# Performance work log

Measured on AMD Instinct MI355X. Metric: run time of the kernel, lower is better.

Reference implementation:

```python
import jax, jax.numpy as jnp
import numpy as np

B, N, FEAT = 4, 100000, 11
NUM_SP = 512  # superpoints per sample
H1, H2, H3, E = 128, 256, 512, 384


def setup_inputs() -> dict:
    key = jax.random.key(0)
    ks = jax.random.split(key, 10)
    s = 0.02
    return {
        "full_features": jax.random.normal(ks[0], (B, N, FEAT), dtype=jnp.float32),
        "full_super_indices": jax.random.randint(ks[1], (B, N), 0, NUM_SP, dtype=jnp.int32),
        "W1": jax.random.normal(ks[2], (H1, FEAT), dtype=jnp.float32) * s,
        "b1": jnp.zeros((H1,), jnp.float32),
        "W2": jax.random.normal(ks[3], (H2, H1), dtype=jnp.float32) * s,
        "b2": jnp.zeros((H2,), jnp.float32),
        "W3": jax.random.normal(ks[4], (H3, H3), dtype=jnp.float32) * s,
        "b3": jnp.zeros((H3,), jnp.float32),
        "W4": jax.random.normal(ks[5], (E, H3), dtype=jnp.float32) * s,
        "b4": jnp.zeros((E,), jnp.float32),
    }


def reference(full_features, full_super_indices, W1, b1, W2, b2, W3, b3, W4, b4):
    # Vectorized form of the per-superpoint mini-PointNet:
    # conv1x1 MLP on points, segment-max pool, concat global+local, MLP, segment-max.
    x = full_features.reshape(B * N, FEAT)
    # first_conv: Conv1d(feat,128,1) -> Conv1d(128,256,1), no activation in between
    h = x @ W1.T + b1
    h = h @ W2.T + b2                                   # [B*N, 256]
    # global segment ids (batch-offset superpoint ids)
    seg = (full_super_indices.astype(jnp.int32) + jnp.arange(B, dtype=jnp.int32)[:, None] * NUM_SP).reshape(-1)
    gmax = jax.ops.segment_max(h, seg, num_segments=B * NUM_SP)  # [B*S, 256]
    g = gmax[seg]                                       # broadcast global feature back to points
    feat = jnp.concatenate([g, h], axis=-1)             # [B*N, 512] (global first, as in torch.cat)
    # second_conv: Conv1d(512,512,1) -> ReLU -> Conv1d(512,E,1)
    y = jax.nn.relu(feat @ W3.T + b3)
    y = y @ W4.T + b4                                   # [B*N, E]
    out = jax.ops.segment_max(y, seg, num_segments=B * NUM_SP)
    return out.reshape(B, NUM_SP, E)
```

## Files before the change

### kernel.cpp

```cpp
#include <hip/hip_runtime.h>
#include <hip/hip_bf16.h>
#include <math.h>

#define BB    4
#define NN    100000
#define NFEAT 11
#define NSP   512
#define NSEG  (BB*NSP)
#define NPTS  (BB*NN)
#define H2    256
#define H3    512
#define EE    384
#define MT    64
#define GS    (MT*8)
#define MI_N  (MT/16)
#define MAXL  15
#define RSEG  512
#define MAXS  12
#define ENCNI 0x007FFFFFu

typedef __attribute__((ext_vector_type(8))) short short8;
typedef __attribute__((ext_vector_type(4))) float f32x4;

__device__ __forceinline__ ushort f2bf(float f) {
  unsigned u = __builtin_bit_cast(unsigned, f);
  unsigned r = (u + 0x7FFFu + ((u >> 16) & 1u)) >> 16;
  return (ushort)r;
}
__device__ __forceinline__ unsigned encf(float f) {
  unsigned u = __builtin_bit_cast(unsigned, f);
  return u ^ ((unsigned)((int)u >> 31) | 0x80000000u);
}
__device__ __forceinline__ float decf(unsigned e) {
  unsigned u = (e & 0x80000000u) ? (e ^ 0x80000000u) : ~e;
  return __builtin_bit_cast(float, u);
}

__global__ void zero_counts(int* __restrict__ counts, int* __restrict__ cursor) {
  int i = blockIdx.x * 256 + threadIdx.x;
  if (i < NSEG) { counts[i] = 0; cursor[i] = 0; }
}

__global__ void prep_init(const float* __restrict__ W1, const float* __restrict__ b1,
                          const float* __restrict__ W2, const float* __restrict__ b2,
                          const float* __restrict__ W3, const float* __restrict__ W4,
                          const int* __restrict__ sidx,
                          float* __restrict__ W12, float* __restrict__ b12,
                          float* __restrict__ W3gT, ushort* __restrict__ W3hP,
                          ushort* __restrict__ W4P,
                          int* __restrict__ counts,
                          unsigned* __restrict__ gmaxEnc, unsigned* __restrict__ out_enc) {
  int u = blockIdx.x * 256 + threadIdx.x;
  if (u < NSEG * EE) out_enc[u] = ENCNI;
  if (u < NSEG * H2) gmaxEnc[u] = ENCNI;
  if (u < NPTS) {
    int seg = sidx[u] + (u / NN) * NSP;
    atomicAdd(&counts[seg], 1);
  }

  if (u < H2 * NFEAT) {
    int c = u / NFEAT, f = u - c * NFEAT;
    float acc = 0.f;
    for (int j = 0; j < 128; ++j) acc += W2[c * 128 + j] * W1[j * NFEAT + f];
    W12[u] = acc;
  } else if (u < 3072) {
    int c = u - H2 * NFEAT;
    float acc = b2[c];
    for (int j = 0; j < 128; ++j) acc += W2[c * 128 + j] * b1[j];
    b12[c] = acc;
  } else if (u < 3072 + 131072) {
    int v = u - 3072;
    int c = v >> 9, o = v & 511;
    W3gT[v] = W3[o * H3 + c];
  } else if (u < 134144 + 16384) {
    int v = u - 134144;
    int ks = v >> 11, rem = v & 2047;
    int nt = rem >> 6, l = rem & 63;
    int n = nt * 16 + (l & 15);
    #pragma unroll
    for (int j = 0; j < 8; ++j) {
      int k = ks * 32 + (l >> 4) * 8 + j;
      W3hP[(size_t)v * 8 + j] = f2bf(W3[n * H3 + H2 + k]);
    }
  } else if (u < 150528 + 24576) {
    int v = u - 150528;
    int ks = v / 1536, rem = v - ks * 1536;
    int nt = rem >> 6, l = rem & 63;
    int n = nt * 16 + (l & 15);
    #pragma unroll
    for (int j = 0; j < 8; ++j) {
      int k = ks * 32 + (l >> 4) * 8 + j;
      W4P[(size_t)v * 8 + j] = f2bf(W4[n * H3 + k]);
    }
  }
}

__global__ void scan_kernel(const int* __restrict__ counts, int* __restrict__ offs) {
  __shared__ int buf[1024];
  int t = threadIdx.x;
  int c0 = counts[2 * t], c1 = counts[2 * t + 1];
  int s = c0 + c1;
  buf[t] = s;
  __syncthreads();
  for (int d = 1; d < 1024; d <<= 1) {
    int add = (t >= d) ? buf[t - d] : 0;
    __syncthreads();
    buf[t] += add;
    __syncthreads();
  }
  int incl = buf[t];
  int excl = incl - s;
  offs[2 * t] = excl;
  offs[2 * t + 1] = excl + c0;
  if (t == 1023) offs[2048] = incl;
}

__global__ void scatter_kernel(const int* __restrict__ sidx, const int* __restrict__ offs,
                               int* __restrict__ cursor, int* __restrict__ perm,
                               int* __restrict__ segp) {
  int i = blockIdx.x * blockDim.x + threadIdx.x;
  if (i < NPTS) {
    int seg = sidx[i] + (i / NN) * NSP;
    int pos = offs[seg] + atomicAdd(&cursor[seg], 1);
    perm[pos] = i;
    segp[pos] = seg;
  }
}

template <bool STOREH>
__global__ __launch_bounds__(512) void gmax_kernel(
    const float* __restrict__ x, const int* __restrict__ perm,
    const int* __restrict__ segp,
    const float* __restrict__ W12, const float* __restrict__ b12,
    unsigned* __restrict__ gmaxEnc, ushort* __restrict__ hG) {
  __shared__ float xs[RSEG * NFEAT];
  __shared__ float W12s[H2 * NFEAT];
  __shared__ float b12s[H2];
  __shared__ int   segd[RSEG];
  __shared__ unsigned gmaxL[MAXS * H2];

  const int t = threadIdx.x;
  const int mbeg = blockIdx.x * RSEG;
  const int nvalid = min(RSEG, NPTS - mbeg);

  for (int u = t; u < RSEG * NFEAT; u += 512) {
    int p = u / NFEAT, f = u - p * NFEAT;
    xs[u] = (p < nvalid) ? x[(size_t)perm[mbeg + p] * NFEAT + f] : 0.f;
  }
  for (int u = t; u < H2 * NFEAT; u += 512) W12s[u] = W12[u];
  if (t < H2) b12s[t] = b12[t];
  segd[t] = (t < nvalid) ? segp[mbeg + t] : segp[mbeg + nvalid - 1];
  for (int u = t; u < MAXS * H2; u += 512) gmaxL[u] = ENCNI;
  __syncthreads();

  const int s_lo = segd[0];
  const int s_hi = segd[nvalid - 1];
  const bool fb = (s_hi - s_lo + 1) > MAXS;

  const int g  = t >> 4;
  const int r0 = t & 15;
  const int cb = g * 8;

  float w12r[8][NFEAT], bbr[8];
  #pragma unroll
  for (int cj = 0; cj < 8; ++cj) {
    bbr[cj] = b12s[cb + cj];
    #pragma unroll
    for (int f = 0; f < NFEAT; ++f) w12r[cj][f] = W12s[(cb + cj) * NFEAT + f];
  }

  float m[8];
  #pragma unroll
  for (int cj = 0; cj < 8; ++cj) m[cj] = -INFINITY;
  int cur = segd[r0];
  bool any = false;

  for (int k = 0; k < 32; ++k) {
    int row = r0 + k * 16;
    if (row >= nvalid) break;
    int sg = segd[row];
    if (sg != cur) {
      #pragma unroll
      for (int cj = 0; cj < 8; ++cj) {
        unsigned e = encf(m[cj]);
        if (fb) atomicMax(&gmaxEnc[(size_t)cur * H2 + cb + cj], e);
        else    atomicMax(&gmaxL[(cur - s_lo) * H2 + cb + cj], e);
      }
      cur = sg;
      #pragma unroll
      for (int cj = 0; cj < 8; ++cj) m[cj] = -INFINITY;
    }
    float acc[8];
    #pragma unroll
    for (int cj = 0; cj < 8; ++cj) acc[cj] = bbr[cj];
    #pragma unroll
    for (int f = 0; f < NFEAT; ++f) {
      float xv = xs[row * NFEAT + f];
      #pragma unroll
      for (int cj = 0; cj < 8; ++cj) acc[cj] += w12r[cj][f] * xv;
    }
    if (STOREH) {
      uint4 pkt;
      pkt.x = (unsigned)f2bf(acc[0]) | ((unsigned)f2bf(acc[1]) << 16);
      pkt.y = (unsigned)f2bf(acc[2]) | ((unsigned)f2bf(acc[3]) << 16);
      pkt.z = (unsigned)f2bf(acc[4]) | ((unsigned)f2bf(acc[5]) << 16);
      pkt.w = (unsigned)f2bf(acc[6]) | ((unsigned)f2bf(acc[7]) << 16);
      int pt = mbeg + row;
      *(uint4*)&hG[(size_t)(pt >> 6) * 16384 + ((size_t)g * 64 + (pt & 63)) * 8] = pkt;
    }
    #pragma unroll
    for (int cj = 0; cj < 8; ++cj) m[cj] = fmaxf(m[cj], acc[cj]);
    any = true;
  }
  if (any) {
    #pragma unroll
    for (int cj = 0; cj < 8; ++cj) {
      unsigned e = encf(m[cj]);
      if (fb) atomicMax(&gmaxEnc[(size_t)cur * H2 + cb + cj], e);
      else    atomicMax(&gmaxL[(cur - s_lo) * H2 + cb + cj], e);
    }
  }

  __syncthreads();
  if (!fb) {
    int nloc = s_hi - s_lo + 1;
    for (int u = t; u < nloc * H2; u += 512) {
      int sg = s_lo + (u >> 8);
      unsigned v = gmaxL[u];
      if (sg > s_lo && sg < s_hi) gmaxEnc[(size_t)sg * H2 + (u & 255)] = v;
      else atomicMax(&gmaxEnc[(size_t)sg * H2 + (u & 255)], v);
    }
  }
}

__global__ __launch_bounds__(256) void gpart_kernel(
    const unsigned* __restrict__ gmaxEnc, const float* __restrict__ W3gT,
    const float* __restrict__ b3, float* __restrict__ gpartG) {
  __shared__ float gm[8 * 256];
  const int t = threadIdx.x;
  const int b = blockIdx.x;
  for (int u = t; u < 8 * 256; u += 256) gm[u] = decf(gmaxEnc[(size_t)b * 8 * 256 + u]);
  __syncthreads();
  const float bb0 = b3[t], bb1 = b3[t + 256];
  float a0[8], a1[8];
  #pragma unroll
  for (int sg = 0; sg < 8; ++sg) { a0[sg] = bb0; a1[sg] = bb1; }
  for (int c = 0; c < 256; ++c) {
    float w0 = W3gT[c * 512 + t], w1 = W3gT[c * 512 + t + 256];
    #pragma unroll
    for (int sg = 0; sg < 8; ++sg) {
      float gv = gm[sg * 256 + c];
      a0[sg] += w0 * gv; a1[sg] += w1 * gv;
    }
  }
  #pragma unroll
  for (int sg = 0; sg < 8; ++sg) {
    size_t s = (size_t)b * 8 + sg;
    gpartG[s * 512 + t] = a0[sg];
    gpartG[s * 512 + t + 256] = a1[sg];
  }
}

__global__ void finalize_kernel(const unsigned* __restrict__ enc, float* __restrict__ out) {
  int i = blockIdx.x * 256 + threadIdx.x;
  if (i < NSEG * EE) out[i] = decf(enc[i]);
}

__global__ __launch_bounds__(512, 4) void main_v4(
    const int* __restrict__ segp, const ushort* __restrict__ hG,
    const ushort* __restrict__ W3hP, const ushort* __restrict__ W4P,
    const float* __restrict__ gpartG, const float* __restrict__ b4,
    unsigned* __restrict__ out_enc) {
  __shared__ __align__(16) ushort hsE[MT * 256];
  __shared__ __align__(16) ushort regB[MT * 256];
  __shared__ int segdL[MT];
  __shared__ int s_loS, nlocS;

  const int t = threadIdx.x;
  const int w = t >> 6;
  const int l = t & 63;
  const int mbeg = blockIdx.x * MT;

  ushort* y1E = regB;
  unsigned* obuf = (unsigned*)regB;

  {
    const size_t tb = (size_t)blockIdx.x * (MT * 256);
    #pragma unroll
    for (int i = 0; i < 4; ++i)
      *(uint4*)&hsE[(size_t)(i * 512 + t) * 8] = *(const uint4*)&hG[tb + (size_t)(i * 512 + t) * 8];
  }
  if (t < MT) segdL[t] = segp[mbeg + t];
  __syncthreads();
  if (t == 0) {
    s_loS = segdL[0];
    nlocS = segdL[MT - 1] - segdL[0] + 1;
  }
  __syncthreads();
  const int s_lo = s_loS;
  const int nloc = nlocS;
  const bool fb = (nloc > MAXL);

  float b4v[3];
  #pragma unroll
  for (int ni = 0; ni < 3; ++ni) b4v[ni] = b4[w * 48 + ni * 16 + (l & 15)];

  int sgr[MI_N][4];
  #pragma unroll
  for (int mi = 0; mi < MI_N; ++mi)
    #pragma unroll
    for (int r = 0; r < 4; ++r)
      sgr[mi][r] = segdL[mi * 16 + (l >> 4) * 4 + r];

  f32x4 acc4[MI_N][3];
  #pragma unroll
  for (int mi = 0; mi < MI_N; ++mi)
    #pragma unroll
    for (int ni = 0; ni < 3; ++ni)
      acc4[mi][ni] = (f32x4){0.f, 0.f, 0.f, 0.f};

  #pragma unroll
  for (int hf = 0; hf < 2; ++hf) {
    f32x4 acc3[MI_N][2];
    #pragma unroll
    for (int mi = 0; mi < MI_N; ++mi)
      #pragma unroll
      for (int ni = 0; ni < 2; ++ni)
        acc3[mi][ni] = (f32x4){0.f, 0.f, 0.f, 0.f};

    float gpv[MI_N][2][4];
    #pragma unroll
    for (int mi = 0; mi < MI_N; ++mi)
      #pragma unroll
      for (int ni = 0; ni < 2; ++ni) {
        int colh = w * 32 + ni * 16 + (l & 15);
        #pragma unroll
        for (int r = 0; r < 4; ++r)
          gpv[mi][ni][r] = gpartG[(size_t)sgr[mi][r] * 512 + hf * 256 + colh];
      }

    #pragma unroll
    for (int ks = 0; ks < 8; ++ks) {
      short8 b0 = *(const short8*)&W3hP[(size_t)((ks * 32 + hf * 16 + w * 2 + 0) * 64 + l) * 8];
      short8 b1 = *(const short8*)&W3hP[(size_t)((ks * 32 + hf * 16 + w * 2 + 1) * 64 + l) * 8];
      #pragma unroll
      for (int mi = 0; mi < MI_N; ++mi) {
        short8 a = *(const short8*)&hsE[(ks * 4 + (l >> 4)) * GS + (mi * 16 + (l & 15)) * 8];
        acc3[mi][0] = __builtin_amdgcn_mfma_f32_16x16x32_bf16(a, b0, acc3[mi][0], 0, 0, 0);
        acc3[mi][1] = __builtin_amdgcn_mfma_f32_16x16x32_bf16(a, b1, acc3[mi][1], 0, 0, 0);
      }
    }

    #pragma unroll
    for (int mi = 0; mi < MI_N; ++mi)
      #pragma unroll
      for (int ni = 0; ni < 2; ++ni) {
        int colh = w * 32 + ni * 16 + (l & 15);
        #pragma unroll
        for (int r = 0; r < 4; ++r) {
          int row = mi * 16 + (l >> 4) * 4 + r;
          float v = fmaxf(acc3[mi][ni][r] + gpv[mi][ni][r], 0.f);
          y1E[(colh >> 3) * GS + row * 8 + (colh & 7)] = f2bf(v);
        }
      }
    __syncthreads();

    #pragma unroll
    for (int ks = 0; ks < 8; ++ks) {
      short8 d0 = *(const short8*)&W4P[(size_t)(((hf * 8 + ks) * 24 + w * 3 + 0) * 64 + l) * 8];
      short8 d1 = *(const short8*)&W4P[(size_t)(((hf * 8 + ks) * 24 + w * 3 + 1) * 64 + l) * 8];
      short8 d2 = *(const short8*)&W4P[(size_t)(((hf * 8 + ks) * 24 + w * 3 + 2) * 64 + l) * 8];
      #pragma unroll
      for (int mi = 0; mi < MI_N; ++mi) {
        short8 a = *(const short8*)&y1E[(ks * 4 + (l >> 4)) * GS + (mi * 16 + (l & 15)) * 8];
        acc4[mi][0] = __builtin_amdgcn_mfma_f32_16x16x32_bf16(a, d0, acc4[mi][0], 0, 0, 0);
        acc4[mi][1] = __builtin_amdgcn_mfma_f32_16x16x32_bf16(a, d1, acc4[mi][1], 0, 0, 0);
        acc4[mi][2] = __builtin_amdgcn_mfma_f32_16x16x32_bf16(a, d2, acc4[mi][2], 0, 0, 0);
      }
    }
    __syncthreads();
  }

  if (!fb) {
    for (int u = t; u < nloc * EE; u += 512) obuf[u] = ENCNI;
    __syncthreads();
    #pragma unroll
    for (int mi = 0; mi < MI_N; ++mi) {
      int sg0 = sgr[mi][0], sg3 = sgr[mi][3];
      #pragma unroll
      for (int ni = 0; ni < 3; ++ni) {
        int col = w * 48 + ni * 16 + (l & 15);
        if (sg0 == sg3) {
          float m4 = fmaxf(fmaxf(acc4[mi][ni][0], acc4[mi][ni][1]),
                           fmaxf(acc4[mi][ni][2], acc4[mi][ni][3]));
          atomicMax(&obuf[(sg0 - s_lo) * EE + col], encf(m4 + b4v[ni]));
        } else {
          #pragma unroll
          for (int r = 0; r < 4; ++r)
            atomicMax(&obuf[(sgr[mi][r] - s_lo) * EE + col],
                      encf(acc4[mi][ni][r] + b4v[ni]));
        }
      }
    }
    __syncthreads();
    for (int u = t; u < nloc * EE; u += 512) {
      unsigned e = obuf[u];
      if (e != ENCNI)
        atomicMax(&out_enc[(size_t)(s_lo + u / EE) * EE + (u % EE)], e);
    }
  } else {
    #pragma unroll
    for (int mi = 0; mi < MI_N; ++mi)
      #pragma unroll
      for (int ni = 0; ni < 3; ++ni) {
        int col = w * 48 + ni * 16 + (l & 15);
        #pragma unroll
        for (int r = 0; r < 4; ++r) {
          unsigned e = encf(acc4[mi][ni][r] + b4v[ni]);
          atomicMax(&out_enc[(size_t)sgr[mi][r] * EE + col], e);
        }
      }
  }
}

__global__ __launch_bounds__(512, 4) void main_kernel(
    const float* __restrict__ x, const int* __restrict__ perm,
    const int* __restrict__ segp,
    const float* __restrict__ W12, const float* __restrict__ b12,
    const ushort* __restrict__ W3hP, const ushort* __restrict__ W4P,
    const float* __restrict__ gpartG, const float* __restrict__ b4,
    unsigned* __restrict__ out_enc) {
  __shared__ __align__(16) ushort hsE[MT * 256];
  __shared__ __align__(16) ushort regB[MT * 256];
  __shared__ float gpartL[MAXL * 256];
  __shared__ int segdL[MT];
  __shared__ int s_loS, nlocS;

  const int t = threadIdx.x;
  const int w = t >> 6;
  const int l = t & 63;
  const int mbeg = blockIdx.x * MT;
  const int nvalid = min(MT, NPTS - mbeg);

  float* xsF  = (float*)regB;
  float* W12s = xsF + 704;
  float* b12s = W12s + 2816;
  ushort* y1E = regB;
  unsigned* obuf = (unsigned*)regB;

  for (int u = t; u < MT * NFEAT; u += 512) {
    int p = u / NFEAT, f = u - p * NFEAT;
    xsF[u] = (p < nvalid) ? x[(size_t)perm[mbeg + p] * NFEAT + f] : 0.f;
  }
  for (int u = t; u < 2816; u += 512) W12s[u] = W12[u];
  if (t < 256) b12s[t] = b12[t];
  if (t < MT) segdL[t] = (t < nvalid) ? segp[mbeg + t] : 0;
  __syncthreads();
  if (t == 0) {
    s_loS = segdL[0];
    nlocS = segdL[nvalid - 1] - segdL[0] + 1;
  }
  __syncthreads();
  const int s_lo = s_loS;
  const int nloc = nlocS;
  const bool fb = (nloc > MAXL);
  if (t < MT && t >= nvalid) segdL[t] = s_lo;

  #pragma unroll
  for (int i = 0; i < 4; ++i) {
    int gran = i * 8 + w;
    int cb = gran * 8;
    int row = l;
    uint4 pkt = {0, 0, 0, 0};
    if (row < nvalid) {
      float acc[8];
      #pragma unroll
      for (int cj = 0; cj < 8; ++cj) acc[cj] = b12s[cb + cj];
      #pragma unroll
      for (int f = 0; f < NFEAT; ++f) {
        float xv = xsF[row * NFEAT + f];
        #pragma unroll
        for (int cj = 0; cj < 8; ++cj) acc[cj] += W12s[(cb + cj) * NFEAT + f] * xv;
      }
      pkt.x = (unsigned)f2bf(acc[0]) | ((unsigned)f2bf(acc[1]) << 16);
      pkt.y = (unsigned)f2bf(acc[2]) | ((unsigned)f2bf(acc[3]) << 16);
      pkt.z = (unsigned)f2bf(acc[4]) | ((unsigned)f2bf(acc[5]) << 16);
      pkt.w = (unsigned)f2bf(acc[6]) | ((unsigned)f2bf(acc[7]) << 16);
    }
    *(uint4*)&hsE[gran * GS + row * 8] = pkt;
  }
  __syncthreads();

  float b4v[3];
  #pragma unroll
  for (int ni = 0; ni < 3; ++ni) b4v[ni] = b4[w * 48 + ni * 16 + (l & 15)];

  f32x4 acc4[MI_N][3];
  #pragma unroll
  for (int mi = 0; mi < MI_N; ++mi)
    #pragma unroll
    for (int ni = 0; ni < 3; ++ni)
      acc4[mi][ni] = (f32x4){0.f, 0.f, 0.f, 0.f};

  #pragma unroll
  for (int hf = 0; hf < 2; ++hf) {
    if (!fb) {
      for (int u = t; u < nloc * 256; u += 512) {
        int sg = u >> 8, c = u & 255;
        gpartL[u] = gpartG[(size_t)(s_lo + sg) * 512 + hf * 256 + c];
      }
    }

    f32x4 acc3[MI_N][2];
    #pragma unroll
    for (int mi = 0; mi < MI_N; ++mi)
      #pragma unroll
      for (int ni = 0; ni < 2; ++ni)
        acc3[mi][ni] = (f32x4){0.f, 0.f, 0.f, 0.f};

    #pragma unroll
    for (int ks = 0; ks < 8; ++ks) {
      short8 b0 = *(const short8*)&W3hP[(size_t)((ks * 32 + hf * 16 + w * 2 + 0) * 64 + l) * 8];
      short8 b1 = *(const short8*)&W3hP[(size_t)((ks * 32 + hf * 16 + w * 2 + 1) * 64 + l) * 8];
      #pragma unroll
      for (int mi = 0; mi < MI_N; ++mi) {
        short8 a = *(const short8*)&hsE[(ks * 4 + (l >> 4)) * GS + (mi * 16 + (l & 15)) * 8];
        acc3[mi][0] = __builtin_amdgcn_mfma_f32_16x16x32_bf16(a, b0, acc3[mi][0], 0, 0, 0);
        acc3[mi][1] = __builtin_amdgcn_mfma_f32_16x16x32_bf16(a, b1, acc3[mi][1], 0, 0, 0);
      }
    }
    __syncthreads();

    #pragma unroll
    for (int mi = 0; mi < MI_N; ++mi)
      #pragma unroll
      for (int ni = 0; ni < 2; ++ni) {
        int colh = w * 32 + ni * 16 + (l & 15);
        #pragma unroll
        for (int r = 0; r < 4; ++r) {
          int row = mi * 16 + (l >> 4) * 4 + r;
          int sg = segdL[row];
          float bias = fb ? gpartG[(size_t)sg * 512 + hf * 256 + colh]
                          : gpartL[(sg - s_lo) * 256 + colh];
          float v = fmaxf(acc3[mi][ni][r] + bias, 0.f);
          y1E[(colh >> 3) * GS + row * 8 + (colh & 7)] = f2bf(v);
        }
      }
    __syncthreads();

    #pragma unroll
    for (int ks = 0; ks < 8; ++ks) {
      short8 d0 = *(const short8*)&W4P[(size_t)(((hf * 8 + ks) * 24 + w * 3 + 0) * 64 + l) * 8];
      short8 d1 = *(const short8*)&W4P[(size_t)(((hf * 8 + ks) * 24 + w * 3 + 1) * 64 + l) * 8];
      short8 d2 = *(const short8*)&W4P[(size_t)(((hf * 8 + ks) * 24 + w * 3 + 2) * 64 + l) * 8];
      #pragma unroll
      for (int mi = 0; mi < MI_N; ++mi) {
        short8 a = *(const short8*)&y1E[(ks * 4 + (l >> 4)) * GS + (mi * 16 + (l & 15)) * 8];
        acc4[mi][0] = __builtin_amdgcn_mfma_f32_16x16x32_bf16(a, d0, acc4[mi][0], 0, 0, 0);
        acc4[mi][1] = __builtin_amdgcn_mfma_f32_16x16x32_bf16(a, d1, acc4[mi][1], 0, 0, 0);
        acc4[mi][2] = __builtin_amdgcn_mfma_f32_16x16x32_bf16(a, d2, acc4[mi][2], 0, 0, 0);
      }
    }
    __syncthreads();
  }

  if (!fb) {
    for (int u = t; u < nloc * EE; u += 512) obuf[u] = ENCNI;
    __syncthreads();
    #pragma unroll
    for (int mi = 0; mi < MI_N; ++mi)
      #pragma unroll
      for (int ni = 0; ni < 3; ++ni) {
        int col = w * 48 + ni * 16 + (l & 15);
        #pragma unroll
        for (int r = 0; r < 4; ++r) {
          int row = mi * 16 + (l >> 4) * 4 + r;
          if (row < nvalid) {
            unsigned e = encf(acc4[mi][ni][r] + b4v[ni]);
            atomicMax(&obuf[(segdL[row] - s_lo) * EE + col], e);
          }
        }
      }
    __syncthreads();
    for (int u = t; u < nloc * EE; u += 512) {
      unsigned e = obuf[u];
      if (e != ENCNI)
        atomicMax(&out_enc[(size_t)(s_lo + u / EE) * EE + (u % EE)], e);
    }
  } else {
    #pragma unroll
    for (int mi = 0; mi < MI_N; ++mi)
      #pragma unroll
      for (int ni = 0; ni < 3; ++ni) {
        int col = w * 48 + ni * 16 + (l & 15);
        #pragma unroll
        for (int r = 0; r < 4; ++r) {
          int row = mi * 16 + (l >> 4) * 4 + r;
          if (row < nvalid) {
            unsigned e = encf(acc4[mi][ni][r] + b4v[ni]);
            atomicMax(&out_enc[(size_t)segdL[row] * EE + col], e);
          }
        }
      }
  }
}

extern "C" void kernel_launch(void* const* d_in, const int* in_sizes, int n_in,
                              void* d_out, int out_size, void* d_ws, size_t ws_size,
                              hipStream_t stream) {
  (void)in_sizes; (void)n_in; (void)out_size;
  const float* x    = (const float*)d_in[0];
  const int*   sidx = (const int*)d_in[1];
  const float* W1   = (const float*)d_in[2];
  const float* b1   = (const float*)d_in[3];
  const float* W2   = (const float*)d_in[4];
  const float* b2   = (const float*)d_in[5];
  const float* W3   = (const float*)d_in[6];
  const float* b3   = (const float*)d_in[7];
  const float* W4   = (const float*)d_in[8];
  const float* b4   = (const float*)d_in[9];
  float* out = (float*)d_out;

  char* ws = (char*)d_ws;
  size_t off = 0;
  auto alloc = [&](size_t bytes) {
    void* p = ws + off;
    off = (off + bytes + 255) & ~(size_t)255;
    return p;
  };
  int*      counts  = (int*)alloc(NSEG * 4);
  int*      cursor  = (int*)alloc(NSEG * 4);
  int*      offs    = (int*)alloc((NSEG + 1) * 4);
  int*      perm    = (int*)alloc((size_t)NPTS * 4);
  int*      segp    = (int*)alloc((size_t)NPTS * 4);
  float*    W12     = (float*)alloc(H2 * NFEAT * 4);
  float*    b12     = (float*)alloc(H2 * 4);
  float*    W3gT    = (float*)alloc((size_t)H2 * H3 * 4);
  ushort*   W3hP    = (ushort*)alloc((size_t)131072 * 2);
  ushort*   W4P     = (ushort*)alloc((size_t)196608 * 2);
  unsigned* gmaxEnc = (unsigned*)alloc((size_t)NSEG * H2 * 4);
  float*    gpartG  = (float*)alloc((size_t)NSEG * H3 * 4);
  unsigned* out_enc = (unsigned*)alloc((size_t)NSEG * EE * 4);
  ushort*   hG      = (ushort*)alloc((size_t)NPTS * 256 * 2);
  const bool useH = (off <= ws_size);

  zero_counts<<<(NSEG + 255) / 256, 256, 0, stream>>>(counts, cursor);
  prep_init<<<(NSEG * EE + 255) / 256, 256, 0, stream>>>(W1, b1, W2, b2, W3, W4, sidx,
                                                         W12, b12, W3gT, W3hP, W4P,
                                                         counts, gmaxEnc, out_enc);
  scan_kernel<<<1, 1024, 0, stream>>>(counts, offs);
  scatter_kernel<<<(NPTS + 255) / 256, 256, 0, stream>>>(sidx, offs, cursor, perm, segp);
  if (useH) {
    gmax_kernel<true><<<(NPTS + RSEG - 1) / RSEG, 512, 0, stream>>>(x, perm, segp, W12, b12, gmaxEnc, hG);
    gpart_kernel<<<NSEG / 8, 256, 0, stream>>>(gmaxEnc, W3gT, b3, gpartG);
    main_v4<<<NPTS / MT, 512, 0, stream>>>(segp, hG, W3hP, W4P, gpartG, b4, out_enc);
  } else {
    gmax_kernel<false><<<(NPTS + RSEG - 1) / RSEG, 512, 0, stream>>>(x, perm, segp, W12, b12, gmaxEnc, hG);
    gpart_kernel<<<NSEG / 8, 256, 0, stream>>>(gmaxEnc, W3gT, b3, gpartG);
    main_kernel<<<NPTS / MT, 512, 0, stream>>>(x, perm, segp, W12, b12,
                                               W3hP, W4P, gpartG, b4, out_enc);
  }
  finalize_kernel<<<(NSEG * EE + 255) / 256, 256, 0, stream>>>(out_enc, out);
}
```

Before: 775.1 us.

## Split W3 stage into four column quarters to cut LDS and registers

The main fused MLP kernel now processes the 512-wide hidden layer in four 128-column chunks instead of two 256-column halves. This shrinks the intermediate LDS buffer and the per-wave accumulators, and raises the launch-bounds occupancy hint from 4 to 6. The global-feature bias is staged per chunk into a small shared table, with a tighter fallback threshold. Per-thread segment-id registers are replaced by LDS reads, and the counts zeroing kernel becomes a memset. The cost is more barriers and more frequent reloading of W4 tiles per chunk.

```diff
diff --git a/kernel.cpp b/kernel.cpp
--- a/kernel.cpp
+++ b/kernel.cpp
@@ -15,6 +15,7 @@
 #define GS    (MT*8)
 #define MI_N  (MT/16)
 #define MAXL  15
+#define MAXL2 10
 #define RSEG  512
 #define MAXS  12
 #define ENCNI 0x007FFFFFu
@@ -34,11 +35,6 @@
 __device__ __forceinline__ float decf(unsigned e) {
   unsigned u = (e & 0x80000000u) ? (e ^ 0x80000000u) : ~e;
   return __builtin_bit_cast(float, u);
-}
-
-__global__ void zero_counts(int* __restrict__ counts, int* __restrict__ cursor) {
-  int i = blockIdx.x * 256 + threadIdx.x;
-  if (i < NSEG) { counts[i] = 0; cursor[i] = 0; }
 }
 
 __global__ void prep_init(const float* __restrict__ W1, const float* __restrict__ b1,
@@ -266,13 +262,14 @@
   if (i < NSEG * EE) out[i] = decf(enc[i]);
 }
 
-__global__ __launch_bounds__(512, 4) void main_v4(
+__global__ __launch_bounds__(512, 6) void main_v5(
     const int* __restrict__ segp, const ushort* __restrict__ hG,
     const ushort* __restrict__ W3hP, const ushort* __restrict__ W4P,
     const float* __restrict__ gpartG, const float* __restrict__ b4,
     unsigned* __restrict__ out_enc) {
   __shared__ __align__(16) ushort hsE[MT * 256];
-  __shared__ __align__(16) ushort regB[MT * 256];
+  __shared__ __align__(16) ushort y1Q[16 * GS];
+  __shared__ float gpartL[MAXL2 * 128];
   __shared__ int segdL[MT];
   __shared__ int s_loS, nlocS;
 
@@ -281,8 +278,7 @@
   const int l = t & 63;
   const int mbeg = blockIdx.x * MT;
 
-  ushort* y1E = regB;
-  unsigned* obuf = (unsigned*)regB;
+  unsigned* obuf = (unsigned*)y1Q;
 
   {
     const size_t tb = (size_t)blockIdx.x * (MT * 256);
@@ -299,18 +295,11 @@
   __syncthreads();
   const int s_lo = s_loS;
   const int nloc = nlocS;
-  const bool fb = (nloc > MAXL);
+  const bool fb = (nloc > MAXL2);
 
   float b4v[3];
   #pragma unroll
   for (int ni = 0; ni < 3; ++ni) b4v[ni] = b4[w * 48 + ni * 16 + (l & 15)];
-
-  int sgr[MI_N][4];
-  #pragma unroll
-  for (int mi = 0; mi < MI_N; ++mi)
-    #pragma unroll
-    for (int r = 0; r < 4; ++r)
-      sgr[mi][r] = segdL[mi * 16 + (l >> 4) * 4 + r];
 
   f32x4 acc4[MI_N][3];
   #pragma unroll
@@ -319,60 +308,52 @@
     for (int ni = 0; ni < 3; ++ni)
       acc4[mi][ni] = (f32x4){0.f, 0.f, 0.f, 0.f};
 
-  #pragma unroll
-  for (int hf = 0; hf < 2; ++hf) {
-    f32x4 acc3[MI_N][2];
-    #pragma unroll
-    for (int mi = 0; mi < MI_N; ++mi)
-      #pragma unroll
-      for (int ni = 0; ni < 2; ++ni)
-        acc3[mi][ni] = (f32x4){0.f, 0.f, 0.f, 0.f};
-
-    float gpv[MI_N][2][4];
-    #pragma unroll
-    for (int mi = 0; mi < MI_N; ++mi)
-      #pragma unroll
-      for (int ni = 0; ni < 2; ++ni) {
-        int colh = w * 32 + ni * 16 + (l & 15);
-        #pragma unroll
-        for (int r = 0; r < 4; ++r)
-          gpv[mi][ni][r] = gpartG[(size_t)sgr[mi][r] * 512 + hf * 256 + colh];
-      }
-
+  const int colq = w * 16 + (l & 15);
+
+  #pragma unroll
+  for (int q = 0; q < 4; ++q) {
+    if (!fb) {
+      for (int u = t; u < nloc * 128; u += 512)
+        gpartL[u] = gpartG[(size_t)(s_lo + (u >> 7)) * 512 + q * 128 + (u & 127)];
+    }
+
+    f32x4 acc3[MI_N];
+    #pragma unroll
+    for (int mi = 0; mi < MI_N; ++mi) acc3[mi] = (f32x4){0.f, 0.f, 0.f, 0.f};
     #pragma unroll
     for (int ks = 0; ks < 8; ++ks) {
-      short8 b0 = *(const short8*)&W3hP[(size_t)((ks * 32 + hf * 16 + w * 2 + 0) * 64 + l) * 8];
-      short8 b1 = *(const short8*)&W3hP[(size_t)((ks * 32 + hf * 16 + w * 2 + 1) * 64 + l) * 8];
+      short8 b0 = *(const short8*)&W3hP[(size_t)((ks * 32 + q * 8 + w) * 64 + l) * 8];
       #pragma unroll
       for (int mi = 0; mi < MI_N; ++mi) {
         short8 a = *(const short8*)&hsE[(ks * 4 + (l >> 4)) * GS + (mi * 16 + (l & 15)) * 8];
-        acc3[mi][0] = __builtin_amdgcn_mfma_f32_16x16x32_bf16(a, b0, acc3[mi][0], 0, 0, 0);
-        acc3[mi][1] = __builtin_amdgcn_mfma_f32_16x16x32_bf16(a, b1, acc3[mi][1], 0, 0, 0);
-      }
-    }
-
-    #pragma unroll
-    for (int mi = 0; mi < MI_N; ++mi)
-      #pragma unroll
-      for (int ni = 0; ni < 2; ++ni) {
-        int colh = w * 32 + ni * 16 + (l & 15);
-        #pragma unroll
-        for (int r = 0; r < 4; ++r) {
-          int row = mi * 16 + (l >> 4) * 4 + r;
-          float v = fmaxf(acc3[mi][ni][r] + gpv[mi][ni][r], 0.f);
-          y1E[(colh >> 3) * GS + row * 8 + (colh & 7)] = f2bf(v);
-        }
-      }
-    __syncthreads();
-
-    #pragma unroll
-    for (int ks = 0; ks < 8; ++ks) {
-      short8 d0 = *(const short8*)&W4P[(size_t)(((hf * 8 + ks) * 24 + w * 3 + 0) * 64 + l) * 8];
-      short8 d1 = *(const short8*)&W4P[(size_t)(((hf * 8 + ks) * 24 + w * 3 + 1) * 64 + l) * 8];
-      short8 d2 = *(const short8*)&W4P[(size_t)(((hf * 8 + ks) * 24 + w * 3 + 2) * 64 + l) * 8];
+        acc3[mi] = __builtin_amdgcn_mfma_f32_16x16x32_bf16(a, b0, acc3[mi], 0, 0, 0);
+      }
+    }
+    __syncthreads();
+
+    #pragma unroll
+    for (int mi = 0; mi < MI_N; ++mi) {
+      #pragma unroll
+      for (int r = 0; r < 4; ++r) {
+        int row = mi * 16 + (l >> 4) * 4 + r;
+        int sg = segdL[row];
+        float bias = fb ? gpartG[(size_t)sg * 512 + q * 128 + colq]
+                        : gpartL[(sg - s_lo) * 128 + colq];
+        float v = fmaxf(acc3[mi][r] + bias, 0.f);
+        y1Q[(colq >> 3) * GS + row * 8 + (colq & 7)] = f2bf(v);
+      }
+    }
+    __syncthreads();
+
+    #pragma unroll
+    for (int ks = 0; ks < 4; ++ks) {
+      int ksg = q * 4 + ks;
+      short8 d0 = *(const short8*)&W4P[(size_t)((ksg * 24 + w * 3 + 0) * 64 + l) * 8];
+      short8 d1 = *(const short8*)&W4P[(size_t)((ksg * 24 + w * 3 + 1) * 64 + l) * 8];
+      short8 d2 = *(const short8*)&W4P[(size_t)((ksg * 24 + w * 3 + 2) * 64 + l) * 8];
       #pragma unroll
       for (int mi = 0; mi < MI_N; ++mi) {
-        short8 a = *(const short8*)&y1E[(ks * 4 + (l >> 4)) * GS + (mi * 16 + (l & 15)) * 8];
+        short8 a = *(const short8*)&y1Q[(ks * 4 + (l >> 4)) * GS + (mi * 16 + (l & 15)) * 8];
         acc4[mi][0] = __builtin_amdgcn_mfma_f32_16x16x32_bf16(a, d0, acc4[mi][0], 0, 0, 0);
         acc4[mi][1] = __builtin_amdgcn_mfma_f32_16x16x32_bf16(a, d1, acc4[mi][1], 0, 0, 0);
         acc4[mi][2] = __builtin_amdgcn_mfma_f32_16x16x32_bf16(a, d2, acc4[mi][2], 0, 0, 0);
@@ -386,7 +367,8 @@
     __syncthreads();
     #pragma unroll
     for (int mi = 0; mi < MI_N; ++mi) {
-      int sg0 = sgr[mi][0], sg3 = sgr[mi][3];
+      int rbase = mi * 16 + (l >> 4) * 4;
+      int sg0 = segdL[rbase], sg3 = segdL[rbase + 3];
       #pragma unroll
       for (int ni = 0; ni < 3; ++ni) {
         int col = w * 48 + ni * 16 + (l & 15);
@@ -397,7 +379,7 @@
         } else {
           #pragma unroll
           for (int r = 0; r < 4; ++r)
-            atomicMax(&obuf[(sgr[mi][r] - s_lo) * EE + col],
+            atomicMax(&obuf[(segdL[rbase + r] - s_lo) * EE + col],
                       encf(acc4[mi][ni][r] + b4v[ni]));
         }
       }
@@ -416,8 +398,9 @@
         int col = w * 48 + ni * 16 + (l & 15);
         #pragma unroll
         for (int r = 0; r < 4; ++r) {
+          int row = mi * 16 + (l >> 4) * 4 + r;
           unsigned e = encf(acc4[mi][ni][r] + b4v[ni]);
-          atomicMax(&out_enc[(size_t)sgr[mi][r] * EE + col], e);
+          atomicMax(&out_enc[(size_t)segdL[row] * EE + col], e);
         }
       }
   }
@@ -644,7 +627,7 @@
   ushort*   hG      = (ushort*)alloc((size_t)NPTS * 256 * 2);
   const bool useH = (off <= ws_size);
 
-  zero_counts<<<(NSEG + 255) / 256, 256, 0, stream>>>(counts, cursor);
+  hipMemsetAsync(counts, 0, (size_t)NSEG * 8, stream);
   prep_init<<<(NSEG * EE + 255) / 256, 256, 0, stream>>>(W1, b1, W2, b2, W3, W4, sidx,
                                                          W12, b12, W3gT, W3hP, W4P,
                                                          counts, gmaxEnc, out_enc);
@@ -653,7 +636,7 @@
   if (useH) {
     gmax_kernel<true><<<(NPTS + RSEG - 1) / RSEG, 512, 0, stream>>>(x, perm, segp, W12, b12, gmaxEnc, hG);
     gpart_kernel<<<NSEG / 8, 256, 0, stream>>>(gmaxEnc, W3gT, b3, gpartG);
-    main_v4<<<NPTS / MT, 512, 0, stream>>>(segp, hG, W3hP, W4P, gpartG, b4, out_enc);
+    main_v5<<<NPTS / MT, 512, 0, stream>>>(segp, hG, W3hP, W4P, gpartG, b4, out_enc);
   } else {
     gmax_kernel<false><<<(NPTS + RSEG - 1) / RSEG, 512, 0, stream>>>(x, perm, segp, W12, b12, gmaxEnc, hG);
     gpart_kernel<<<NSEG / 8, 256, 0, stream>>>(gmaxEnc, W3gT, b3, gpartG);
```

Measured after the change: 979.7 us. 1.26x slower.
